# Performance work log

Measured on AMD Instinct MI355X. Metric: run time of the kernel, lower is better.

## Reference

```python
import jax, jax.numpy as jnp
import numpy as np

N_NODES = 50000
N_EDGES = 800000
F_IN, F_LAT, F_OUT = 64, 64, 64


def _graph_conv(x, W, b, src, dst, deg_out_isqrt, deg_in_isqrt):
    # DGL GraphConv, norm='both': D_out^{-1/2} scaling on src side,
    # linear transform (mult-first since in_feats >= out_feats),
    # scatter-sum to dst, D_in^{-1/2} scaling on dst side, + bias.
    n = x.shape[0]
    h = (x * deg_out_isqrt[:, None]) @ W              # [N, F_out]
    msg = h[src]                                      # [E, F_out] gather
    agg = jax.ops.segment_sum(msg, dst, num_segments=n)  # [N, F_out] scatter
    return agg * deg_in_isqrt[:, None] + b


def setup_inputs() -> dict:
    key = jax.random.key(0)
    ks = jax.random.split(key, 6)
    x = jax.random.normal(ks[0], (N_NODES, F_IN), dtype=jnp.float32)
    W1 = jax.random.normal(ks[1], (F_IN, F_LAT), dtype=jnp.float32) / np.sqrt(F_IN)
    b1 = jnp.zeros((F_LAT,), dtype=jnp.float32)
    W2 = jax.random.normal(ks[2], (F_LAT, F_OUT), dtype=jnp.float32) / np.sqrt(F_LAT)
    b2 = jnp.zeros((F_OUT,), dtype=jnp.float32)
    src = jax.random.randint(ks[3], (N_EDGES,), 0, N_NODES, dtype=jnp.int32)
    dst = jax.random.randint(ks[4], (N_EDGES,), 0, N_NODES, dtype=jnp.int32)
    return {"x": x, "W1": W1, "b1": b1, "W2": W2, "b2": b2, "src": src, "dst": dst}


def reference(x, W1, b1, W2, b2, src, dst):
    n = x.shape[0]
    ones = jnp.ones((src.shape[0],), dtype=x.dtype)
    deg_out = jax.ops.segment_sum(ones, src, num_segments=n)
    deg_in = jax.ops.segment_sum(ones, dst, num_segments=n)
    deg_out_isqrt = jnp.where(deg_out > 0, jax.lax.rsqrt(jnp.maximum(deg_out, 1.0)), 0.0)
    deg_in_isqrt = jnp.where(deg_in > 0, jax.lax.rsqrt(jnp.maximum(deg_in, 1.0)), 0.0)
    h = _graph_conv(x, W1, b1, src, dst, deg_out_isqrt, deg_in_isqrt)
    h = jax.nn.relu(h)
    out = _graph_conv(h, W2, b2, src, dst, deg_out_isqrt, deg_in_isqrt)
    return out
```

## Files before the change

### kernel.cpp

```cpp
#include <hip/hip_runtime.h>

#define NF 64
#define BC 32
#define RANGE 8192

typedef __attribute__((ext_vector_type(8))) short short8;
typedef __attribute__((ext_vector_type(4))) float floatx4;

__device__ __forceinline__ unsigned short f2bf(float f) {
  unsigned int u = __float_as_uint(f);
  return (unsigned short)((u + 0x7fffu + ((u >> 16) & 1u)) >> 16);
}

__global__ __launch_bounds__(256) void hist_kernel(
    const int* __restrict__ src, const int* __restrict__ dst,
    unsigned short* __restrict__ Gout, unsigned short* __restrict__ Gin,
    unsigned char* __restrict__ rank, int n, int nE, int R) {
  __shared__ int cnt[RANGE];
  const int rb = blockIdx.x % (R * BC);
  const int kind = blockIdx.x / (R * BC);
  const int r = rb / BC, b = rb % BC;
  const int r0 = r * RANGE;
  for (int i = threadIdx.x; i < RANGE; i += 256) cnt[i] = 0;
  __syncthreads();
  const int chunk = (nE + BC - 1) / BC;
  const int lo = b * chunk, hi = min(lo + chunk, nE);
  if (kind == 0) {
    for (int e = lo + threadIdx.x; e < hi; e += 256) {
      unsigned int k = (unsigned int)(dst[e] - r0);
      if (k < (unsigned int)RANGE) {
        int old = atomicAdd(&cnt[k], 1);
        rank[e] = (unsigned char)old;
      }
    }
    __syncthreads();
    for (int i = threadIdx.x; i < RANGE; i += 256) {
      int nidx = r0 + i;
      if (nidx < n) Gin[(size_t)b * n + nidx] = (unsigned short)cnt[i];
    }
  } else {
    for (int e = lo + threadIdx.x; e < hi; e += 256) {
      unsigned int k = (unsigned int)(src[e] - r0);
      if (k < (unsigned int)RANGE) atomicAdd(&cnt[k], 1);
    }
    __syncthreads();
    for (int i = threadIdx.x; i < RANGE; i += 256) {
      int nidx = r0 + i;
      if (nidx < n) Gout[(size_t)b * n + nidx] = (unsigned short)cnt[i];
    }
  }
}

__global__ __launch_bounds__(256) void colscan_scan1_kernel(
    unsigned short* __restrict__ Gin, const unsigned short* __restrict__ Gout,
    int* __restrict__ deg_in, int* __restrict__ deg_out,
    int* __restrict__ lscan, int* __restrict__ bsum, int n) {
  __shared__ int s[256];
  const int tid = threadIdx.x;
  const int i = blockIdx.x * 256 + tid;
  int di = 0;
  if (i < n) {
    int base = 0;
    #pragma unroll 8
    for (int b = 0; b < BC; ++b) {
      int c = Gin[(size_t)b * n + i];
      Gin[(size_t)b * n + i] = (unsigned short)base;
      base += c;
    }
    di = base;
    int dsum = 0;
    #pragma unroll 8
    for (int b = 0; b < BC; ++b) dsum += Gout[(size_t)b * n + i];
    deg_in[i] = di;
    deg_out[i] = dsum;
  }
  s[tid] = di;
  __syncthreads();
  #pragma unroll
  for (int off = 1; off < 256; off <<= 1) {
    int t2 = (tid >= off) ? s[tid - off] : 0;
    __syncthreads();
    s[tid] += t2;
    __syncthreads();
  }
  if (i < n) lscan[i] = s[tid] - di;
  if (tid == 255) bsum[blockIdx.x] = s[255];
}

__global__ __launch_bounds__(256) void scan3_kernel(
    const int* __restrict__ lscan, const int* __restrict__ bsum,
    const int* __restrict__ deg_out, const int* __restrict__ deg_in,
    const unsigned short* __restrict__ Gin, int* __restrict__ base,
    int* __restrict__ row_start, float* __restrict__ so, float* __restrict__ si,
    int n, int nE) {
  __shared__ int red[256];
  const int tid = threadIdx.x;
  const int b = blockIdx.x;
  red[tid] = (tid < b) ? bsum[tid] : 0;
  __syncthreads();
  #pragma unroll
  for (int s = 128; s > 0; s >>= 1) {
    if (tid < s) red[tid] += red[tid + s];
    __syncthreads();
  }
  const int off = red[0];
  const int i = b * 256 + tid;
  if (b == 0 && tid == 0) row_start[n] = nE;
  if (i < n) {
    int rs = lscan[i] + off;
    row_start[i] = rs;
    int dO = deg_out[i];
    int dI = deg_in[i];
    so[i] = dO > 0 ? rsqrtf((float)dO) : 0.f;
    si[i] = dI > 0 ? rsqrtf((float)dI) : 0.f;
    #pragma unroll 8
    for (int c = 0; c < BC; ++c)
      base[(size_t)c * n + i] = rs + (int)Gin[(size_t)c * n + i];
  }
}

__global__ __launch_bounds__(256) void place_kernel(
    const int* __restrict__ src, const int* __restrict__ dst,
    const unsigned char* __restrict__ rank, const int* __restrict__ base,
    unsigned short* __restrict__ sorted, int n, int nE, int chunk) {
  int e = blockIdx.x * 256 + threadIdx.x;
  if (e >= nE) return;
  int d = dst[e];
  int b = e / chunk;
  int pos = base[(size_t)b * n + d] + (int)rank[e];
  sorted[pos] = (unsigned short)src[e];
}

__device__ __forceinline__ void mfma_gemm_core(
    const unsigned short* __restrict__ Ab, const unsigned short* __restrict__ Wt,
    unsigned short* __restrict__ H, int row0, int n, int t) {
  const int w = t >> 6, lane = t & 63;
  const int quad = lane >> 4, l15 = lane & 15;
  const short8 a0 = *(const short8*)&Ab[(w * 16 + l15) * 72 + quad * 8];
  const short8 a1 = *(const short8*)&Ab[(w * 16 + l15) * 72 + 32 + quad * 8];
  #pragma unroll
  for (int cg = 0; cg < 4; ++cg) {
    const short8 b0 = *(const short8*)&Wt[(cg * 16 + l15) * 72 + quad * 8];
    const short8 b1 = *(const short8*)&Wt[(cg * 16 + l15) * 72 + 32 + quad * 8];
    floatx4 acc = {0.f, 0.f, 0.f, 0.f};
    acc = __builtin_amdgcn_mfma_f32_16x16x32_bf16(a0, b0, acc, 0, 0, 0);
    acc = __builtin_amdgcn_mfma_f32_16x16x32_bf16(a1, b1, acc, 0, 0, 0);
    #pragma unroll
    for (int reg = 0; reg < 4; ++reg) {
      int grow = row0 + w * 16 + quad * 4 + reg;
      if (grow < n) H[(size_t)grow * NF + cg * 16 + l15] = f2bf(acc[reg]);
    }
  }
}

__device__ __forceinline__ void stage_wt(
    const float* __restrict__ W, unsigned short* __restrict__ Wt, int t) {
  #pragma unroll
  for (int i = 0; i < 16; ++i) {
    int idx = t + 256 * i;
    int k = idx >> 6, j = idx & 63;
    Wt[j * 72 + k] = f2bf(W[idx]);
  }
}

__global__ __launch_bounds__(256) void gemm1_kernel(
    const float* __restrict__ A, const float* __restrict__ so,
    const float* __restrict__ W, unsigned short* __restrict__ H, int n) {
  __shared__ __align__(16) unsigned short Ab[64 * 72];
  __shared__ __align__(16) unsigned short Wt[64 * 72];
  const int t = threadIdx.x;
  stage_wt(W, Wt, t);
  const int row0 = blockIdx.x * 64;
  #pragma unroll
  for (int i = 0; i < 4; ++i) {
    int idx = t + 256 * i;
    int r = idx >> 4, c4 = idx & 15;
    int gr = row0 + r;
    float4 v = {0.f, 0.f, 0.f, 0.f};
    float s = 0.f;
    if (gr < n) {
      v = *(const float4*)&A[(size_t)gr * NF + c4 * 4];
      s = so[gr];
    }
    ushort4 o;
    o.x = f2bf(v.x * s); o.y = f2bf(v.y * s);
    o.z = f2bf(v.z * s); o.w = f2bf(v.w * s);
    *(ushort4*)&Ab[r * 72 + c4 * 4] = o;
  }
  __syncthreads();
  mfma_gemm_core(Ab, Wt, H, row0, n, t);
}

__global__ __launch_bounds__(256) void gemm2_kernel(
    const unsigned short* __restrict__ Tb, const float* __restrict__ W,
    unsigned short* __restrict__ H, int n) {
  __shared__ __align__(16) unsigned short Ab[64 * 72];
  __shared__ __align__(16) unsigned short Wt[64 * 72];
  const int t = threadIdx.x;
  stage_wt(W, Wt, t);
  const int row0 = blockIdx.x * 64;
  #pragma unroll
  for (int i = 0; i < 4; ++i) {
    int idx = t + 256 * i;
    int r = idx >> 4, c4 = idx & 15;
    int gr = row0 + r;
    ushort4 v = {0, 0, 0, 0};
    if (gr < n) v = *(const ushort4*)&Tb[(size_t)gr * NF + c4 * 4];
    *(ushort4*)&Ab[r * 72 + c4 * 4] = v;
  }
  __syncthreads();
  mfma_gemm_core(Ab, Wt, H, row0, n, t);
}

__device__ __forceinline__ void gather_sum(
    const unsigned short* __restrict__ H, const unsigned short* __restrict__ srcs,
    int beg, int end, int g, int c, float* acc) {
  const float4* Hv = (const float4*)H;
  int e = beg;
  for (; e + 16 <= end; e += 16) {
    int ia = srcs[e + g];
    int ib = srcs[e + 8 + g];
    float4 va = Hv[(size_t)ia * 8 + c];
    float4 vb = Hv[(size_t)ib * 8 + c];
    const unsigned int* pa = (const unsigned int*)&va;
    const unsigned int* pb = (const unsigned int*)&vb;
    #pragma unroll
    for (int k = 0; k < 4; ++k) {
      acc[2 * k]     += __uint_as_float(pa[k] << 16) + __uint_as_float(pb[k] << 16);
      acc[2 * k + 1] += __uint_as_float(pa[k] & 0xffff0000u) + __uint_as_float(pb[k] & 0xffff0000u);
    }
  }
  if (e + 8 <= end) {
    int ia = srcs[e + g];
    float4 va = Hv[(size_t)ia * 8 + c];
    const unsigned int* pa = (const unsigned int*)&va;
    #pragma unroll
    for (int k = 0; k < 4; ++k) {
      acc[2 * k]     += __uint_as_float(pa[k] << 16);
      acc[2 * k + 1] += __uint_as_float(pa[k] & 0xffff0000u);
    }
    e += 8;
  }
  if (e < end) {
    int idx = (e + g < end) ? (e + g) : (end - 1);
    float m = (e + g < end) ? 1.f : 0.f;
    int ia = srcs[idx];
    float4 va = Hv[(size_t)ia * 8 + c];
    const unsigned int* pa = (const unsigned int*)&va;
    #pragma unroll
    for (int k = 0; k < 4; ++k) {
      acc[2 * k]     += m * __uint_as_float(pa[k] << 16);
      acc[2 * k + 1] += m * __uint_as_float(pa[k] & 0xffff0000u);
    }
  }
  #pragma unroll
  for (int d = 8; d <= 32; d <<= 1) {
    #pragma unroll
    for (int k = 0; k < 8; ++k) acc[k] += __shfl_xor(acc[k], d);
  }
}

__global__ __launch_bounds__(256) void agg1_kernel(
    const unsigned short* __restrict__ H1, const int* __restrict__ row_start,
    const unsigned short* __restrict__ srcs, const float* __restrict__ si,
    const float* __restrict__ so, const float* __restrict__ b1,
    unsigned short* __restrict__ T, int n) {
  int node = blockIdx.x * 4 + (threadIdx.x >> 6);
  if (node >= n) return;
  const int lane = threadIdx.x & 63;
  const int g = lane >> 3;
  const int c = lane & 7;
  float acc[8] = {0, 0, 0, 0, 0, 0, 0, 0};
  gather_sum(H1, srcs, row_start[node], row_start[node + 1], g, c, acc);
  if (g == 0) {
    const float sin = si[node];
    const float son = so[node];
    ushort4 o0, o1;
    float v;
    v = fmaxf(fmaf(acc[0], sin, b1[c * 8 + 0]), 0.f) * son; o0.x = f2bf(v);
    v = fmaxf(fmaf(acc[1], sin, b1[c * 8 + 1]), 0.f) * son; o0.y = f2bf(v);
    v = fmaxf(fmaf(acc[2], sin, b1[c * 8 + 2]), 0.f) * son; o0.z = f2bf(v);
    v = fmaxf(fmaf(acc[3], sin, b1[c * 8 + 3]), 0.f) * son; o0.w = f2bf(v);
    v = fmaxf(fmaf(acc[4], sin, b1[c * 8 + 4]), 0.f) * son; o1.x = f2bf(v);
    v = fmaxf(fmaf(acc[5], sin, b1[c * 8 + 5]), 0.f) * son; o1.y = f2bf(v);
    v = fmaxf(fmaf(acc[6], sin, b1[c * 8 + 6]), 0.f) * son; o1.z = f2bf(v);
    v = fmaxf(fmaf(acc[7], sin, b1[c * 8 + 7]), 0.f) * son; o1.w = f2bf(v);
    *(ushort4*)&T[(size_t)node * NF + c * 8]     = o0;
    *(ushort4*)&T[(size_t)node * NF + c * 8 + 4] = o1;
  }
}

__global__ __launch_bounds__(256) void agg2_kernel(
    const unsigned short* __restrict__ H2, const int* __restrict__ row_start,
    const unsigned short* __restrict__ srcs, const float* __restrict__ si,
    const float* __restrict__ b2, float* __restrict__ out, int n) {
  int node = blockIdx.x * 4 + (threadIdx.x >> 6);
  if (node >= n) return;
  const int lane = threadIdx.x & 63;
  const int g = lane >> 3;
  const int c = lane & 7;
  float acc[8] = {0, 0, 0, 0, 0, 0, 0, 0};
  gather_sum(H2, srcs, row_start[node], row_start[node + 1], g, c, acc);
  if (g == 0) {
    const float sin = si[node];
    const float4 b4a = *(const float4*)&b2[c * 8];
    const float4 b4b = *(const float4*)&b2[c * 8 + 4];
    float4 r0, r1;
    r0.x = fmaf(acc[0], sin, b4a.x);
    r0.y = fmaf(acc[1], sin, b4a.y);
    r0.z = fmaf(acc[2], sin, b4a.z);
    r0.w = fmaf(acc[3], sin, b4a.w);
    r1.x = fmaf(acc[4], sin, b4b.x);
    r1.y = fmaf(acc[5], sin, b4b.y);
    r1.z = fmaf(acc[6], sin, b4b.z);
    r1.w = fmaf(acc[7], sin, b4b.w);
    *(float4*)&out[(size_t)node * NF + c * 8]     = r0;
    *(float4*)&out[(size_t)node * NF + c * 8 + 4] = r1;
  }
}

extern "C" void kernel_launch(void* const* d_in, const int* in_sizes, int n_in,
                              void* d_out, int out_size, void* d_ws, size_t ws_size,
                              hipStream_t stream) {
  const float* x  = (const float*)d_in[0];
  const float* W1 = (const float*)d_in[1];
  const float* b1 = (const float*)d_in[2];
  const float* W2 = (const float*)d_in[3];
  const float* b2 = (const float*)d_in[4];
  const int* src  = (const int*)d_in[5];
  const int* dst  = (const int*)d_in[6];
  float* out = (float*)d_out;

  const int N = in_sizes[0] / NF;
  const int E = in_sizes[5];
  const int NB = (N + 255) / 256;
  const int R  = (N + RANGE - 1) / RANGE;
  const int CH = (E + BC - 1) / BC;

  char* ws = (char*)d_ws;
  size_t p = 0;
  auto alloc = [&](size_t bytes) -> void* {
    void* r = ws + p;
    p = (p + bytes + 255) & ~(size_t)255;
    return r;
  };
  int*   deg_out_i  = (int*)  alloc((size_t)N * 4);
  int*   deg_in_i   = (int*)  alloc((size_t)N * 4);
  float* so         = (float*)alloc((size_t)N * 4);
  float* si         = (float*)alloc((size_t)N * 4);
  int*   row_start  = (int*)  alloc((size_t)(N + 1) * 4);
  int*   bsum       = (int*)  alloc((size_t)NB * 4);
  int*   lscan      = (int*)  alloc((size_t)N * 4);
  unsigned short* sorted_u16 = (unsigned short*)alloc((size_t)E * 2);
  unsigned short* h1   = (unsigned short*)alloc((size_t)N * NF * 2);
  unsigned short* tb   = (unsigned short*)alloc((size_t)N * NF * 2);
  unsigned short* G_in  = (unsigned short*)alloc((size_t)BC * N * 2);
  unsigned short* G_out = (unsigned short*)alloc((size_t)BC * N * 2);
  unsigned char*  rank  = (unsigned char*)alloc((size_t)E);
  int*            base  = (int*)alloc((size_t)BC * N * 4);
  unsigned short* h2 = h1;

  hist_kernel<<<2 * R * BC, 256, 0, stream>>>(src, dst, G_out, G_in, rank, N, E, R);

  colscan_scan1_kernel<<<NB, 256, 0, stream>>>(G_in, G_out, deg_in_i, deg_out_i,
                                               lscan, bsum, N);

  scan3_kernel<<<NB, 256, 0, stream>>>(lscan, bsum, deg_out_i, deg_in_i,
                                       G_in, base, row_start, so, si, N, E);

  place_kernel<<<(E + 255) / 256, 256, 0, stream>>>(src, dst, rank, base,
                                                    sorted_u16, N, E, CH);

  const int ggrid = (N + 63) / 64;
  const int agrid = (N + 3) / 4;

  gemm1_kernel<<<ggrid, 256, 0, stream>>>(x, so, W1, h1, N);

  agg1_kernel<<<agrid, 256, 0, stream>>>(h1, row_start, sorted_u16, si, so, b1, tb, N);

  gemm2_kernel<<<ggrid, 256, 0, stream>>>(tb, W2, h2, N);

  agg2_kernel<<<agrid, 256, 0, stream>>>(h2, row_start, sorted_u16, si, b2, out, N);
}
```

Baseline: 197.8 us.

## Fuse edge placement into gemm1, vectorize histogram loads, alias base buffer

The separate place kernel is merged into the first GEMM launch as extra blocks, which removes a kernel launch and lets the scatter overlap with the GEMM work. The histogram kernel now reads keys as int4 with a scalar tail. The chunk size is rounded to a multiple of four so those vector loads stay aligned. The edge-block count doubles from 32 to 64, which gives more parallelism in the histogram but makes the column scan read and write more per-block count data. The large per-block base array now reuses the tb buffer. It spills into the G_out region that follows it, which is safe only because G_out is dead by then.

```diff
diff --git a/kernel.cpp b/kernel.cpp
--- a/kernel.cpp
+++ b/kernel.cpp
@@ -1,7 +1,7 @@
 #include <hip/hip_runtime.h>
 
 #define NF 64
-#define BC 32
+#define BC 64
 #define RANGE 8192
 
 typedef __attribute__((ext_vector_type(8))) short short8;
@@ -15,7 +15,7 @@
 __global__ __launch_bounds__(256) void hist_kernel(
     const int* __restrict__ src, const int* __restrict__ dst,
     unsigned short* __restrict__ Gout, unsigned short* __restrict__ Gin,
-    unsigned char* __restrict__ rank, int n, int nE, int R) {
+    unsigned char* __restrict__ rank, int n, int nE, int R, int chunk) {
   __shared__ int cnt[RANGE];
   const int rb = blockIdx.x % (R * BC);
   const int kind = blockIdx.x / (R * BC);
@@ -23,15 +23,28 @@
   const int r0 = r * RANGE;
   for (int i = threadIdx.x; i < RANGE; i += 256) cnt[i] = 0;
   __syncthreads();
-  const int chunk = (nE + BC - 1) / BC;
   const int lo = b * chunk, hi = min(lo + chunk, nE);
+  if (hi <= lo) return;
+  const int* keys = kind ? src : dst;
+  const int n4 = (hi - lo) >> 2;
+  const int4* keys4 = (const int4*)(keys + lo);
   if (kind == 0) {
-    for (int e = lo + threadIdx.x; e < hi; e += 256) {
-      unsigned int k = (unsigned int)(dst[e] - r0);
-      if (k < (unsigned int)RANGE) {
-        int old = atomicAdd(&cnt[k], 1);
-        rank[e] = (unsigned char)old;
-      }
+    for (int i = threadIdx.x; i < n4; i += 256) {
+      int4 v = keys4[i];
+      int e0 = lo + 4 * i;
+      unsigned int k;
+      k = (unsigned int)(v.x - r0);
+      if (k < (unsigned int)RANGE) rank[e0 + 0] = (unsigned char)atomicAdd(&cnt[k], 1);
+      k = (unsigned int)(v.y - r0);
+      if (k < (unsigned int)RANGE) rank[e0 + 1] = (unsigned char)atomicAdd(&cnt[k], 1);
+      k = (unsigned int)(v.z - r0);
+      if (k < (unsigned int)RANGE) rank[e0 + 2] = (unsigned char)atomicAdd(&cnt[k], 1);
+      k = (unsigned int)(v.w - r0);
+      if (k < (unsigned int)RANGE) rank[e0 + 3] = (unsigned char)atomicAdd(&cnt[k], 1);
+    }
+    for (int e = lo + 4 * n4 + threadIdx.x; e < hi; e += 256) {
+      unsigned int k = (unsigned int)(keys[e] - r0);
+      if (k < (unsigned int)RANGE) rank[e] = (unsigned char)atomicAdd(&cnt[k], 1);
     }
     __syncthreads();
     for (int i = threadIdx.x; i < RANGE; i += 256) {
@@ -39,8 +52,20 @@
       if (nidx < n) Gin[(size_t)b * n + nidx] = (unsigned short)cnt[i];
     }
   } else {
-    for (int e = lo + threadIdx.x; e < hi; e += 256) {
-      unsigned int k = (unsigned int)(src[e] - r0);
+    for (int i = threadIdx.x; i < n4; i += 256) {
+      int4 v = keys4[i];
+      unsigned int k;
+      k = (unsigned int)(v.x - r0);
+      if (k < (unsigned int)RANGE) atomicAdd(&cnt[k], 1);
+      k = (unsigned int)(v.y - r0);
+      if (k < (unsigned int)RANGE) atomicAdd(&cnt[k], 1);
+      k = (unsigned int)(v.z - r0);
+      if (k < (unsigned int)RANGE) atomicAdd(&cnt[k], 1);
+      k = (unsigned int)(v.w - r0);
+      if (k < (unsigned int)RANGE) atomicAdd(&cnt[k], 1);
+    }
+    for (int e = lo + 4 * n4 + threadIdx.x; e < hi; e += 256) {
+      unsigned int k = (unsigned int)(keys[e] - r0);
       if (k < (unsigned int)RANGE) atomicAdd(&cnt[k], 1);
     }
     __syncthreads();
@@ -119,18 +144,6 @@
   }
 }
 
-__global__ __launch_bounds__(256) void place_kernel(
-    const int* __restrict__ src, const int* __restrict__ dst,
-    const unsigned char* __restrict__ rank, const int* __restrict__ base,
-    unsigned short* __restrict__ sorted, int n, int nE, int chunk) {
-  int e = blockIdx.x * 256 + threadIdx.x;
-  if (e >= nE) return;
-  int d = dst[e];
-  int b = e / chunk;
-  int pos = base[(size_t)b * n + d] + (int)rank[e];
-  sorted[pos] = (unsigned short)src[e];
-}
-
 __device__ __forceinline__ void mfma_gemm_core(
     const unsigned short* __restrict__ Ab, const unsigned short* __restrict__ Wt,
     unsigned short* __restrict__ H, int row0, int n, int t) {
@@ -163,12 +176,24 @@
   }
 }
 
-__global__ __launch_bounds__(256) void gemm1_kernel(
+__global__ __launch_bounds__(256) void place_gemm1_kernel(
     const float* __restrict__ A, const float* __restrict__ so,
-    const float* __restrict__ W, unsigned short* __restrict__ H, int n) {
+    const float* __restrict__ W, unsigned short* __restrict__ H, int n, int ggrid,
+    const int* __restrict__ src, const int* __restrict__ dst,
+    const unsigned char* __restrict__ rank, const int* __restrict__ base,
+    unsigned short* __restrict__ sorted, int nE, int chunk) {
   __shared__ __align__(16) unsigned short Ab[64 * 72];
   __shared__ __align__(16) unsigned short Wt[64 * 72];
   const int t = threadIdx.x;
+  if ((int)blockIdx.x >= ggrid) {
+    int e = (blockIdx.x - ggrid) * 256 + t;
+    if (e < nE) {
+      int d = dst[e];
+      int b = e / chunk;
+      sorted[base[(size_t)b * n + d] + (int)rank[e]] = (unsigned short)src[e];
+    }
+    return;
+  }
   stage_wt(W, Wt, t);
   const int row0 = blockIdx.x * 64;
   #pragma unroll
@@ -335,7 +360,7 @@
   const int E = in_sizes[5];
   const int NB = (N + 255) / 256;
   const int R  = (N + RANGE - 1) / RANGE;
-  const int CH = (E + BC - 1) / BC;
+  const int CH = (((E + BC - 1) / BC) + 3) & ~3;
 
   char* ws = (char*)d_ws;
   size_t p = 0;
@@ -352,15 +377,16 @@
   int*   bsum       = (int*)  alloc((size_t)NB * 4);
   int*   lscan      = (int*)  alloc((size_t)N * 4);
   unsigned short* sorted_u16 = (unsigned short*)alloc((size_t)E * 2);
-  unsigned short* h1   = (unsigned short*)alloc((size_t)N * NF * 2);
-  unsigned short* tb   = (unsigned short*)alloc((size_t)N * NF * 2);
+  unsigned char*  rank  = (unsigned char*)alloc((size_t)E);
+  unsigned short* h1    = (unsigned short*)alloc((size_t)N * NF * 2);
   unsigned short* G_in  = (unsigned short*)alloc((size_t)BC * N * 2);
+  unsigned short* tb    = (unsigned short*)alloc((size_t)N * NF * 2);
   unsigned short* G_out = (unsigned short*)alloc((size_t)BC * N * 2);
-  unsigned char*  rank  = (unsigned char*)alloc((size_t)E);
-  int*            base  = (int*)alloc((size_t)BC * N * 4);
+  int* base = (int*)tb;
   unsigned short* h2 = h1;
 
-  hist_kernel<<<2 * R * BC, 256, 0, stream>>>(src, dst, G_out, G_in, rank, N, E, R);
+  hist_kernel<<<2 * R * BC, 256, 0, stream>>>(src, dst, G_out, G_in, rank,
+                                              N, E, R, CH);
 
   colscan_scan1_kernel<<<NB, 256, 0, stream>>>(G_in, G_out, deg_in_i, deg_out_i,
                                                lscan, bsum, N);
@@ -368,13 +394,12 @@
   scan3_kernel<<<NB, 256, 0, stream>>>(lscan, bsum, deg_out_i, deg_in_i,
                                        G_in, base, row_start, so, si, N, E);
 
-  place_kernel<<<(E + 255) / 256, 256, 0, stream>>>(src, dst, rank, base,
-                                                    sorted_u16, N, E, CH);
-
   const int ggrid = (N + 63) / 64;
+  const int pgrid = (E + 255) / 256;
   const int agrid = (N + 3) / 4;
 
-  gemm1_kernel<<<ggrid, 256, 0, stream>>>(x, so, W1, h1, N);
+  place_gemm1_kernel<<<ggrid + pgrid, 256, 0, stream>>>(
+      x, so, W1, h1, N, ggrid, src, dst, rank, base, sorted_u16, E, CH);
 
   agg1_kernel<<<agrid, 256, 0, stream>>>(h1, row_start, sorted_u16, si, so, b1, tb, N);
 
```

Result: faster. 185.1 us (-6.4%).
